# Kernel optimization log

Measured on AMD Instinct MI355X. Metric: run time of the kernel, lower is better.

## Reference

```python
import jax, jax.numpy as jnp
import numpy as np

# my_conv from Sufficient-Vision-Transformer: unfold + per-channel weighted sums
# over k*k patch positions (two weight sets), concat, interleave channels, add bias.
# This is exactly a depthwise conv with 2 filters per input channel, output
# channels interleaved as [res1_0, res2_0, res1_1, res2_1, ...].

K = 3       # kernel_size
PAD = 1     # padding
STRIDE = 1  # stride


def setup_inputs() -> dict:
    key = jax.random.key(0)
    k1, k2, k3, k4 = jax.random.split(key, 4)
    B, C, H, W = 32, 192, 56, 56
    x = jax.random.normal(k1, (B, C, H, W), dtype=jnp.float32)
    weight1 = jax.random.normal(k2, (1, 1, C, K * K), dtype=jnp.float32)
    weight2 = jax.random.normal(k3, (1, 1, C, K * K), dtype=jnp.float32)
    bias = jax.random.normal(k4, (1, 2 * C, 1, 1), dtype=jnp.float32)
    return {"x": x, "weight1": weight1, "weight2": weight2, "bias": bias}


def reference(x, weight1, weight2, bias):
    B, C, H, W = x.shape
    # torch Unfold orders patch rows channel-major, kernel positions row-major
    # (kh, kw) -> matches reshape of weight (C, k*k) -> (C, 1, k, k).
    w1 = weight1.reshape(C, 1, K, K)
    w2 = weight2.reshape(C, 1, K, K)
    # Interleave filters per group: group i -> output channels [2i, 2i+1]
    # with feature_group_count=C; reproduces order_list = [0, C, 1, C+1, ...].
    w = jnp.stack([w1, w2], axis=1).reshape(2 * C, 1, K, K)
    out = jax.lax.conv_general_dilated(
        x, w,
        window_strides=(STRIDE, STRIDE),
        padding=[(PAD, PAD), (PAD, PAD)],
        feature_group_count=C,
        dimension_numbers=("NCHW", "OIHW", "NCHW"),
    )
    return out + bias
```

## Files before the change

### kernel.cpp

```cpp
#include <hip/hip_runtime.h>


#define BB 32
#define CC 192
#define HH 56
#define WW 56
#define W4 (WW / 4)

__global__ __launch_bounds__(256) void dwconv2_kernel(
    const float* __restrict__ x,
    const float* __restrict__ w1,
    const float* __restrict__ w2,
    const float* __restrict__ bias,
    float* __restrict__ out)
{
    const int total = BB * CC * HH * W4;
    int idx = blockIdx.x * blockDim.x + threadIdx.x;
    if (idx >= total) return;

    int w4 = idx % W4;
    int t  = idx / W4;
    int h  = t % HH;
    t /= HH;
    int c  = t % CC;
    int b  = t / CC;

    float a1[9], a2[9];
#pragma unroll
    for (int i = 0; i < 9; ++i) {
        a1[i] = w1[c * 9 + i];
        a2[i] = w2[c * 9 + i];
    }
    const float bias1 = bias[2 * c];
    const float bias2 = bias[2 * c + 1];

    const float* xp = x + ((size_t)(b * CC + c) * HH) * WW;
    const int w0 = w4 * 4;

    float row[3][6];
#pragma unroll
    for (int r = 0; r < 3; ++r) {
        int hh = h - 1 + r;
        bool hv = (hh >= 0) && (hh < HH);
        const float* rp = xp + hh * WW + w0;
        float4 mid = hv ? *(const float4*)rp : make_float4(0.f, 0.f, 0.f, 0.f);
        float left  = (hv && w0 > 0)        ? rp[-1] : 0.f;
        float right = (hv && (w0 + 4) < WW) ? rp[4]  : 0.f;
        row[r][0] = left;
        row[r][1] = mid.x;
        row[r][2] = mid.y;
        row[r][3] = mid.z;
        row[r][4] = mid.w;
        row[r][5] = right;
    }

    float o1[4], o2[4];
#pragma unroll
    for (int p = 0; p < 4; ++p) {
        float s1 = bias1, s2 = bias2;
#pragma unroll
        for (int r = 0; r < 3; ++r) {
#pragma unroll
            for (int kc = 0; kc < 3; ++kc) {
                float v = row[r][p + kc];
                s1 += v * a1[r * 3 + kc];
                s2 += v * a2[r * 3 + kc];
            }
        }
        o1[p] = s1;
        o2[p] = s2;
    }

    float* op = out + (((size_t)(b * 2 * CC + 2 * c) * HH + h) * WW + w0);
    *(float4*)op = make_float4(o1[0], o1[1], o1[2], o1[3]);
    *(float4*)(op + (size_t)HH * WW) = make_float4(o2[0], o2[1], o2[2], o2[3]);
}

extern "C" void kernel_launch(void* const* d_in, const int* in_sizes, int n_in,
                              void* d_out, int out_size, void* d_ws, size_t ws_size,
                              hipStream_t stream) {
    const float* x  = (const float*)d_in[0];
    const float* w1 = (const float*)d_in[1];
    const float* w2 = (const float*)d_in[2];
    const float* bs = (const float*)d_in[3];
    float* out = (float*)d_out;

    const int total = BB * CC * HH * W4;
    const int block = 256;
    const int grid = (total + block - 1) / block;
    dwconv2_kernel<<<grid, block, 0, stream>>>(x, w1, w2, bs, out);
}
```

Before: 249.2 us.

## Stage each channel plane in LDS with one block per (batch, channel)

```diff
diff --git a/kernel.cpp b/kernel.cpp
--- a/kernel.cpp
+++ b/kernel.cpp
@@ -5,75 +5,76 @@
 #define CC 192
 #define HH 56
 #define WW 56
-#define W4 (WW / 4)
+#define W4 14
+#define PITCH 60
+#define LROWS 58
 
-__global__ __launch_bounds__(256) void dwconv2_kernel(
+typedef float f32x4 __attribute__((ext_vector_type(4)));
+
+__global__ __launch_bounds__(784) void dwconv2_lds_kernel(
     const float* __restrict__ x,
     const float* __restrict__ w1,
     const float* __restrict__ w2,
     const float* __restrict__ bias,
     float* __restrict__ out)
 {
-    const int total = BB * CC * HH * W4;
-    int idx = blockIdx.x * blockDim.x + threadIdx.x;
-    if (idx >= total) return;
+    __shared__ float tile[LROWS * PITCH];
+    __shared__ float wts[20];
 
-    int w4 = idx % W4;
-    int t  = idx / W4;
-    int h  = t % HH;
-    t /= HH;
-    int c  = t % CC;
-    int b  = t / CC;
+    const int bc = blockIdx.x;
+    const int c  = bc % CC;
+
+    const int t  = threadIdx.x;
+    const int h  = t / W4;
+    const int w4 = t % W4;
+    const int w0 = w4 * 4;
+
+    if (t < 9)        wts[t]      = w1[c * 9 + t];
+    else if (t < 18)  wts[t]      = w2[c * 9 + (t - 9)];
+    else if (t < 20)  wts[t]      = bias[2 * c + (t - 18)];
+
+    if (t < 60)            tile[t] = 0.f;
+    else if (t < 120)      tile[57 * PITCH + (t - 60)] = 0.f;
+    else if (t < 176)      tile[(t - 119) * PITCH] = 0.f;
+    else if (t < 232)      tile[(t - 175) * PITCH + 57] = 0.f;
+
+    const f32x4 v = __builtin_nontemporal_load(
+        (const f32x4*)(x + ((size_t)bc * HH + h) * WW + w0));
+    float* dst = &tile[(h + 1) * PITCH + 1 + w0];
+    dst[0] = v.x; dst[1] = v.y; dst[2] = v.z; dst[3] = v.w;
+
+    __syncthreads();
 
     float a1[9], a2[9];
 #pragma unroll
-    for (int i = 0; i < 9; ++i) {
-        a1[i] = w1[c * 9 + i];
-        a2[i] = w2[c * 9 + i];
-    }
-    const float bias1 = bias[2 * c];
-    const float bias2 = bias[2 * c + 1];
-
-    const float* xp = x + ((size_t)(b * CC + c) * HH) * WW;
-    const int w0 = w4 * 4;
-
-    float row[3][6];
-#pragma unroll
-    for (int r = 0; r < 3; ++r) {
-        int hh = h - 1 + r;
-        bool hv = (hh >= 0) && (hh < HH);
-        const float* rp = xp + hh * WW + w0;
-        float4 mid = hv ? *(const float4*)rp : make_float4(0.f, 0.f, 0.f, 0.f);
-        float left  = (hv && w0 > 0)        ? rp[-1] : 0.f;
-        float right = (hv && (w0 + 4) < WW) ? rp[4]  : 0.f;
-        row[r][0] = left;
-        row[r][1] = mid.x;
-        row[r][2] = mid.y;
-        row[r][3] = mid.z;
-        row[r][4] = mid.w;
-        row[r][5] = right;
-    }
+    for (int i = 0; i < 9; ++i) { a1[i] = wts[i]; a2[i] = wts[9 + i]; }
+    const float bias1 = wts[18], bias2 = wts[19];
 
     float o1[4], o2[4];
 #pragma unroll
-    for (int p = 0; p < 4; ++p) {
-        float s1 = bias1, s2 = bias2;
+    for (int p = 0; p < 4; ++p) { o1[p] = bias1; o2[p] = bias2; }
+
 #pragma unroll
-        for (int r = 0; r < 3; ++r) {
+    for (int r = 0; r < 3; ++r) {
+        const float* rp = &tile[(h + r) * PITCH + w0];
+        float rv[6];
+#pragma unroll
+        for (int j = 0; j < 6; ++j) rv[j] = rp[j];
+#pragma unroll
+        for (int p = 0; p < 4; ++p) {
 #pragma unroll
             for (int kc = 0; kc < 3; ++kc) {
-                float v = row[r][p + kc];
-                s1 += v * a1[r * 3 + kc];
-                s2 += v * a2[r * 3 + kc];
+                o1[p] += rv[p + kc] * a1[r * 3 + kc];
+                o2[p] += rv[p + kc] * a2[r * 3 + kc];
             }
         }
-        o1[p] = s1;
-        o2[p] = s2;
     }
 
-    float* op = out + (((size_t)(b * 2 * CC + 2 * c) * HH + h) * WW + w0);
-    *(float4*)op = make_float4(o1[0], o1[1], o1[2], o1[3]);
-    *(float4*)(op + (size_t)HH * WW) = make_float4(o2[0], o2[1], o2[2], o2[3]);
+    const size_t obase = (((size_t)(bc * 2) * HH) + h) * WW + w0;
+    f32x4 s1; s1.x = o1[0]; s1.y = o1[1]; s1.z = o1[2]; s1.w = o1[3];
+    f32x4 s2; s2.x = o2[0]; s2.y = o2[1]; s2.z = o2[2]; s2.w = o2[3];
+    __builtin_nontemporal_store(s1, (f32x4*)(out + obase));
+    __builtin_nontemporal_store(s2, (f32x4*)(out + obase + (size_t)HH * WW));
 }
 
 extern "C" void kernel_launch(void* const* d_in, const int* in_sizes, int n_in,
@@ -85,8 +86,5 @@
     const float* bs = (const float*)d_in[3];
     float* out = (float*)d_out;
 
-    const int total = BB * CC * HH * W4;
-    const int block = 256;
-    const int grid = (total + block - 1) / block;
-    dwconv2_kernel<<<grid, block, 0, stream>>>(x, w1, w2, bs, out);
+    dwconv2_lds_kernel<<<BB * CC, 784, 0, stream>>>(x, w1, w2, bs, out);
 }
```

Result: faster. 239.1 us (-4.0%).
